# Performance work log

Measured on AMD Instinct MI355X. Metric: run time of the kernel, lower is better.

## Reference

```python
import jax, jax.numpy as jnp
import numpy as np

# Static config (mirrors XMem wrapper schedule)
B, T, H, W = 2, 16, 512, 512
P = 16                      # pad_divide_by(16) / stride-16 key encoder
h, w = H // P, W // P
HW = h * w
CK, CF, CV, CH = 64, 256, 512, 64   # key dim == hidden dim (XMem), f16 feat dim, value dim
MEM_EVERY, DEEP_EVERY = 5, 10
EPS = 1e-6


def setup_inputs() -> dict:
    key = jax.random.key(0)
    ks = jax.random.split(key, 12)
    def g(k, shape, s=0.02):
        return jax.random.normal(k, shape, jnp.float32) * s
    return {
        "frames": jax.random.normal(ks[0], (B, T, 3, H, W), jnp.float32),
        "init_masks": jax.random.uniform(ks[1], (B, 1, H, W), jnp.float32),
        "init_labels": jnp.ones((B, 1), jnp.int32),
        # key encoder (stride-16 patchify + linear projections, KeyProjection style)
        "W_key": g(ks[2], (3 * P * P, CK)),
        "W_shr": g(ks[3], (3 * P * P, 1)),
        "W_sel": g(ks[4], (3 * P * P, CK)),
        "W_f16": g(ks[5], (3 * P * P, CF)),
        # value encoder: concat(f16, mask) -> value; hidden update
        "W_val": g(ks[6], (CF + 1, CV)),
        "W_hid2": g(ks[7], (CV + CH, CH)),
        # decoder: concat(f16, readout, hidden) -> new hidden; -> fg logit
        "W_hd": g(ks[8], (CF + CV + CH, CH)),
        "W_dec": g(ks[9], (CF + CV + CH, 1)),
    }


def _patchify(img):  # [3,H,W] -> [HW, 3*P*P]
    x = img.reshape(3, h, P, w, P).transpose(1, 3, 0, 2, 4)
    return x.reshape(HW, 3 * P * P)


def _down(m):  # [H,W] -> [HW], average-pool by P (value-encoder mask downsample)
    return m.reshape(h, P, w, P).mean(axis=(1, 3)).reshape(HW)


def _aggregate(prob):  # XMem aggregate: prob [K,H,W] -> softmax([bg, fg...]) [K+1,H,W]
    bg = jnp.prod(1.0 - prob, axis=0, keepdims=True)
    newp = jnp.clip(jnp.concatenate([bg, prob], 0), 1e-7, 1.0 - 1e-7)
    logits = jnp.log(newp / (1.0 - newp))
    return jax.nn.softmax(logits, axis=0)


def _match(mk, ms, mv, qk, qe):
    # XMem get_similarity with shrinkage (ms) and selection (qe):
    # mk [CK,N], ms [N], mv [CV,N], qk/qe [CK,HW]
    a_sq = jnp.einsum('cn,cp->np', mk * mk, qe)
    two_ab = 2.0 * jnp.einsum('cn,cp->np', mk, qk * qe)
    b_sq = (qe * qk * qk).sum(0)                       # [HW]
    sim = (-a_sq + two_ab - b_sq) * ms[:, None] / np.sqrt(CK)
    aff = jax.nn.softmax(sim, axis=0)                  # softmax over memory entries
    return mv @ aff                                    # [CV, HW]


def _run_seq(frames_b, m0, Wk, Wsh, Wse, Wf, Wv, Wh2, Whd, Wdec):
    # frames_b [T,3,H,W], m0 [1,H,W]. H,W divisible by 16 so pad_divide_by is identity.
    patches = jax.vmap(_patchify)(frames_b)            # [T,HW,768]
    keys = patches @ Wk                                # [T,HW,CK]
    shrs = (patches @ Wsh) ** 2 + 1.0                  # [T,HW,1]  (d_proj**2 + 1)
    sels = jax.nn.sigmoid(patches @ Wse)               # [T,HW,CK]
    f16s = patches @ Wf                                # [T,HW,CF]

    mem_k, mem_s, mem_v = [], [], []
    hidden = jnp.zeros((HW, CH), jnp.float32)          # create_hidden_state
    last_mem, last_deep = 0, -DEEP_EVERY
    feats, masks = [], []
    for t in range(T):  # static schedule: mem frames and deep updates depend only on t
        is_mem = (t - last_mem >= MEM_EVERY or t == 0) and t != T - 1
        is_deep = (t - last_deep >= DEEP_EVERY) and t != T - 1
        qk, qe, f16 = keys[t].T, sels[t].T, f16s[t]    # qk,qe [CK,HW]
        ms_t = shrs[t][:, 0]
        pred_prob = None
        if t > 0:  # need_segment
            mk = jnp.concatenate(mem_k, 1)
            msv = jnp.concatenate(mem_s, 0)
            mv = jnp.concatenate(mem_v, 1)
            readout = _match(mk, msv, mv, qk, qe).T    # [HW,CV]
            hidden_local = jnp.tanh(jnp.concatenate([f16, readout, hidden], 1) @ Whd)
            fg = jnp.concatenate([f16, readout, hidden_local], 1) @ Wdec  # [HW,1]
            logits = jnp.concatenate([jnp.zeros((HW, 1), jnp.float32), fg], 1)
            pred_prob = jax.nn.softmax(logits, 1).T    # [2,HW] with bg
            if t != T - 1:                             # is_normal_update
                hidden = hidden_local
            m = pred_prob[1]
            feat = (hidden_local * m[:, None]).sum(0) / jnp.maximum(m.sum(), EPS)
            union = jax.image.resize(pred_prob[1].reshape(h, w), (H, W), 'bilinear')
        else:
            feat = keys[t].mean(0)                     # key.mean over spatial
            union = jnp.zeros((H, W), jnp.float32)
        feats.append(feat)
        masks.append(union)
        if is_mem:
            if t == 0:
                wprob = _aggregate(m0)                 # [2,H,W]
                wmask = _down(jax.lax.stop_gradient(wprob[1]))
            else:
                wmask = jax.lax.stop_gradient(pred_prob[1])
            value = jnp.concatenate([f16, wmask[:, None]], 1) @ Wv      # [HW,CV]
            hidden2 = jnp.tanh(jnp.concatenate([value, hidden], 1) @ Wh2)
            mem_k.append(qk)
            mem_s.append(ms_t)
            mem_v.append(value.T)
            last_mem = t
            if is_deep:
                hidden = hidden2
                last_deep = t
    return jnp.stack(feats, 0)                         # [T,CH]


def reference(frames, init_masks, init_labels, W_key, W_shr, W_sel, W_f16,
              W_val, W_hid2, W_hd, W_dec):
    del init_labels  # single-object labels [1]; no math
    run = lambda fb, mb: _run_seq(fb, mb, W_key, W_shr, W_sel, W_f16,
                                  W_val, W_hid2, W_hd, W_dec)
    return jax.vmap(run)(frames, init_masks)           # [B,T,CH]
```

## Files before the change

### kernel.cpp

```cpp
#include <hip/hip_runtime.h>
#include <cstdint>

typedef __bf16 bf16_t;
typedef __attribute__((ext_vector_type(8))) __bf16 bf16x8;
typedef __attribute__((ext_vector_type(4))) __bf16 bf16x4;
typedef __attribute__((ext_vector_type(4))) float f32x4;

#define MFMA16(a,b,c) __builtin_amdgcn_mfma_f32_16x16x32_bf16((a),(b),(c),0,0,0)

constexpr size_t PVSTR   = (size_t)2*5*1024*72;
constexpr size_t o_wcatT = 0;
constexpr size_t o_whfT  = o_wcatT + 172032;
constexpr size_t o_wvhT  = o_whfT  + 16384;
constexpr size_t o_wvh1  = o_wvhT  + 10240;
constexpr size_t o_WvT   = o_wvh1  + 80;
constexpr size_t o_whh   = o_WvT   + 65536;
constexpr size_t o_wh2T  = o_whh   + 4224;
constexpr size_t o_keyb  = o_wh2T  + 18432;
constexpr size_t o_ms    = o_keyb  + 1048576;
constexpr size_t o_qeb   = o_ms    + 32768;
constexpr size_t o_f16b  = o_qeb   + 1048576;
constexpr size_t o_qfb   = o_f16b  + 4194304;
constexpr size_t o_kfb   = o_qfb   + 2621440;
constexpr size_t o_vb    = o_kfb   + 491520;
constexpr size_t o_vhT   = o_vb    + 1572864;
constexpr size_t o_pv    = o_vhT   + 393216;
constexpr size_t o_p16   = o_pv    + 12*PVSTR;
constexpr size_t o_mh    = o_p16   + 1179648;
constexpr size_t o_hid   = o_mh    + 2027520;
constexpr size_t o_wmk   = o_hid   + 131072;
constexpr size_t ws_need = o_wmk   + 2048;

__global__ __launch_bounds__(256)
void k_init(const float* __restrict__ Wk, const float* __restrict__ Wsh,
            const float* __restrict__ Wse, const float* __restrict__ Wf,
            const float* __restrict__ Wv, const float* __restrict__ Wh2,
            const float* __restrict__ Whd, const float* __restrict__ Wdec,
            bf16_t* __restrict__ wcatT, bf16_t* __restrict__ whfT,
            bf16_t* __restrict__ WvT, float* __restrict__ whh,
            bf16_t* __restrict__ wh2T, float* __restrict__ out,
            bf16_t* __restrict__ wvhT, float* __restrict__ wvh1)
{
    int idx = blockIdx.x*256 + threadIdx.x;
    if (idx < 344064) {
        int n = idx/768, k = idx%768;
        float v = 0.f;
        if (n < 64)       v = Wk[k*64+n];
        else if (n == 64) v = Wsh[k];
        else if (n < 129) v = Wse[k*64+(n-65)];
        else if (n < 385) v = Wf[k*256+(n-129)];
        wcatT[idx] = (bf16_t)v;
        return;
    }
    idx -= 344064;
    if (idx < 32768) {
        int c = idx/256, k = idx%256;
        float v = 0.f;
        if (c < 64) v = Whd[k*64+c]; else if (c == 64) v = Wdec[k];
        whfT[idx] = (bf16_t)v;
        return;
    }
    idx -= 32768;
    if (idx < 131072) {
        int n = idx/256, k = idx%256;
        WvT[idx] = (bf16_t)Wv[k*512+n];
        return;
    }
    idx -= 131072;
    if (idx < 4224) {
        int k = idx/66, c = idx%66;
        float v = 0.f;
        if (c < 64) v = Whd[(768+k)*64+c]; else if (c == 64) v = Wdec[768+k];
        whh[idx] = v;
        return;
    }
    idx -= 4224;
    if (idx < 36864) {
        int c = idx/576, k = idx%576;
        wh2T[idx] = (bf16_t)Wh2[k*64+c];
        return;
    }
    idx -= 36864;
    if (idx < 128) {
        int b = idx>>6, c = idx&63;
        out[(size_t)b*1024 + c] = 0.f;
        return;
    }
    idx -= 128;
    if (idx < 20480) {
        int k = idx / 80, c = idx % 80;
        float s = 0.f;
        if (c < 65) {
            for (int j = 0; j < 512; j++) {
                float hv = (c < 64) ? Whd[(256+j)*64 + c] : Wdec[256 + j];
                s = fmaf(Wv[k*512 + j], hv, s);
            }
        }
        wvhT[(size_t)c*256 + k] = (bf16_t)s;
        return;
    }
    idx -= 20480;
    if (idx < 65) {
        int c = idx;
        float s = 0.f;
        for (int j = 0; j < 512; j++) {
            float hv = (c < 64) ? Whd[(256+j)*64 + c] : Wdec[256 + j];
            s = fmaf(Wv[256*512 + j], hv, s);
        }
        wvh1[c] = s;
    }
}

__global__ __launch_bounds__(512)
void k_proj(const float* __restrict__ frames, const bf16_t* __restrict__ wcatT,
            bf16_t* __restrict__ keyb, float* __restrict__ msb,
            bf16_t* __restrict__ qeb, bf16_t* __restrict__ f16b)
{
    const int bx = blockIdx.x, bt = blockIdx.y;
    const int p0 = bx*64;
    const int tid = threadIdx.x, lane = tid & 63, w = tid >> 6;
    const int wp = w >> 2, wn = w & 3;
    const int l15 = lane & 15, l4 = lane >> 4;
    __shared__ __align__(16) bf16_t Al[2][4][512];
    f32x4 acc[2][7] = {};
    const float* fb = frames + (size_t)bt*786432;

    const int lr = tid >> 7, lxb = (tid & 127)*8;
    const float* gbase = fb + (size_t)((bx*2 + (lr>>1))*16 + (lr&1))*512 + (tid & 127)*4;
    const int wbyte = lr*1024 + (lxb ^ (((lxb>>7)&3)<<4));
    const int rb_in = l15*32 + (l4&1)*16;
    const int rbyte = (wp*2 + (l4>>1))*1024 + (rb_in ^ (((rb_in>>7)&3)<<4));
    char* lds = (char*)&Al[0][0][0];

    #define PLOAD(dst, kc) dst = *(const float4*)(gbase + (size_t)((kc)>>3)*262144 + (size_t)(((kc)&7)*2)*512)
    #define PSTORE(buf, v) { bf16x4 pk; pk[0]=(bf16_t)(v).x; pk[1]=(bf16_t)(v).y; \
        pk[2]=(bf16_t)(v).z; pk[3]=(bf16_t)(v).w; \
        *(bf16x4*)(lds + (buf)*4096 + wbyte) = pk; }
    #define LBAR() { asm volatile("s_waitcnt lgkmcnt(0)" ::: "memory"); \
        __builtin_amdgcn_sched_barrier(0); \
        __builtin_amdgcn_s_barrier(); \
        __builtin_amdgcn_sched_barrier(0); }

    float4 va, vb;
    PLOAD(va, 0); PLOAD(vb, 1);
    PSTORE(0, va); PLOAD(va, 2);
    PSTORE(1, vb); PLOAD(vb, 3);
    LBAR();

    for (int kc = 0; kc < 24; kc++) {
        const int buf = kc & 1;
        bf16x8 af0 = *(const bf16x8*)(lds + buf*4096 + rbyte);
        bf16x8 af1 = *(const bf16x8*)(lds + buf*4096 + rbyte + 512);
        LBAR();
        if (kc < 22) {
            if (buf == 0) { PSTORE(0, va); if (kc < 20) PLOAD(va, kc+4); }
            else          { PSTORE(1, vb); if (kc < 20) PLOAD(vb, kc+4); }
        }
        #pragma unroll
        for (int fj = 0; fj < 7; fj++) {
            int n = wn*112 + fj*16 + l15;
            bf16x8 bv = *(const bf16x8*)(wcatT + (size_t)n*768 + kc*32 + l4*8);
            acc[0][fj] = MFMA16(af0, bv, acc[0][fj]);
            acc[1][fj] = MFMA16(af1, bv, acc[1][fj]);
        }
    }
    #undef PLOAD
    #undef PSTORE
    #undef LBAR

    #pragma unroll
    for (int fi = 0; fi < 2; fi++)
    #pragma unroll
    for (int fj = 0; fj < 7; fj++) {
        int nn = wn*112 + fj*16 + l15;
        #pragma unroll
        for (int rr = 0; rr < 4; rr++) {
            int pp = p0 + wp*32 + fi*16 + l4*4 + rr;
            float v = acc[fi][fj][rr];
            size_t rowb = (size_t)bt*1024 + pp;
            if (nn < 64)       keyb[rowb*64 + nn] = (bf16_t)v;
            else if (nn == 64) msb[rowb] = v*v + 1.f;
            else if (nn < 129) qeb[rowb*64 + (nn-65)] = (bf16_t)(1.f/(1.f+expf(-v)));
            else if (nn < 385) f16b[rowb*256 + (nn-129)] = (bf16_t)v;
        }
    }
}

__global__ __launch_bounds__(512)
void k_qf(const bf16_t* __restrict__ keyb, const bf16_t* __restrict__ qeb,
          bf16_t* __restrict__ qfb, float* __restrict__ out)
{
    int bt = blockIdx.x;
    int p = blockIdx.y*8 + threadIdx.y;
    int c = threadIdx.x;
    size_t rowb = (size_t)bt*1024 + p;
    float qk = (float)keyb[rowb*64 + c];
    float qv = (float)qeb[rowb*64 + c];
    float bsq = qv*qk*qk;
    #pragma unroll
    for (int off = 32; off; off >>= 1) bsq += __shfl_xor(bsq, off);
    bf16_t* q = qfb + rowb*160;
    q[c]      = (bf16_t)(qv*qk);
    q[64 + c] = (bf16_t)qv;
    if (c == 0) q[128] = (bf16_t)bsq;
    if (c < 31) q[129 + c] = (bf16_t)0.f;
    if ((bt & 15) == 0) {
        __shared__ float fred[64];
        if (threadIdx.y == 0) fred[c] = 0.f;
        __syncthreads();
        atomicAdd(&fred[c], qk);
        __syncthreads();
        if (threadIdx.y == 0)
            atomicAdd(&out[(size_t)(bt >> 4)*1024 + c], fred[c]*(1.f/1024.f));
    }
}

__global__ __launch_bounds__(256)
void k_mask0(const float* __restrict__ im, float* __restrict__ wmask)
{
    int blk = blockIdx.x;
    int b = blk >> 5, i = blk & 31;
    int tid = threadIdx.x;
    int xq = tid & 127, yh = tid >> 7;
    const float* base = im + (size_t)b*262144 + (size_t)(i*16)*512;
    float s = 0.f;
    for (int yy = 0; yy < 8; yy++) {
        int y = yy*2 + yh;
        float4 v = *(const float4*)(base + (size_t)y*512 + xq*4);
        float e[4] = {v.x, v.y, v.z, v.w};
        #pragma unroll
        for (int u = 0; u < 4; u++) {
            float pc = fminf(fmaxf(e[u],      1e-7f), 1.f-1e-7f);
            float qc = fminf(fmaxf(1.f-e[u],  1e-7f), 1.f-1e-7f);
            s += pc*pc/(pc*pc + qc*qc);
        }
    }
    __shared__ float red[32];
    if (tid < 32) red[tid] = 0.f;
    __syncthreads();
    atomicAdd(&red[xq >> 2], s);
    __syncthreads();
    if (tid < 32) wmask[b*1024 + i*32 + tid] = red[tid]*(1.f/256.f);
}

__global__ __launch_bounds__(128)
void k_prep(const bf16_t* __restrict__ f16b, const bf16_t* __restrict__ keyb,
            const float* __restrict__ msb, const float* __restrict__ wmk,
            const bf16_t* __restrict__ wvhT, const float* __restrict__ wvh1,
            bf16_t* __restrict__ kfb, bf16_t* __restrict__ vhT, int tm, int slot)
{
    int b = blockIdx.y, n0 = blockIdx.x*32;
    int tid = threadIdx.x, lane = tid & 63, w = tid >> 6;
    {
        int row = n0 + (tid >> 2), q = tid & 3;
        size_t rowb = (size_t)(b*16 + tm)*1024 + row;
        float m = msb[rowb];
        bf16_t* kr = kfb + ((size_t)b*3072 + slot*1024 + row)*160;
        bf16x8 k0v = *(const bf16x8*)(keyb + rowb*64 + q*16);
        bf16x8 k1v = *(const bf16x8*)(keyb + rowb*64 + q*16 + 8);
        bf16x8 o0, o1, s0, s1;
        #pragma unroll
        for (int u = 0; u < 8; u++) {
            float mk0 = (float)k0v[u], mk1 = (float)k1v[u];
            o0[u] = (bf16_t)( m*mk0*0.25f);       o1[u] = (bf16_t)( m*mk1*0.25f);
            s0[u] = (bf16_t)(-m*mk0*mk0*0.125f);  s1[u] = (bf16_t)(-m*mk1*mk1*0.125f);
        }
        *(bf16x8*)(kr + q*16)      = o0;  *(bf16x8*)(kr + q*16 + 8)      = o1;
        *(bf16x8*)(kr + 64 + q*16) = s0;  *(bf16x8*)(kr + 64 + q*16 + 8) = s1;
        if (q == 0) kr[128] = (bf16_t)(-m*0.125f);
        else if (q == 1) { for (int u = 0; u < 15; u++) kr[129+u] = (bf16_t)0.f; }
        else if (q == 2) { for (int u = 0; u < 16; u++) kr[144+u] = (bf16_t)0.f; }
    }
    int l15 = lane & 15, l4 = lane >> 4;
    const bf16_t* A = f16b + ((size_t)(b*16 + tm)*1024 + n0 + w*16 + l15)*256;
    f32x4 acc[5] = {};
    #pragma unroll
    for (int ks = 0; ks < 8; ks++) {
        bf16x8 a0 = *(const bf16x8*)(A + ks*32 + l4*8);
        #pragma unroll
        for (int cf = 0; cf < 5; cf++) {
            bf16x8 bv = *(const bf16x8*)(wvhT + (size_t)(cf*16 + l15)*256 + ks*32 + l4*8);
            acc[cf] = MFMA16(a0, bv, acc[cf]);
        }
    }
    #pragma unroll
    for (int cf = 0; cf < 5; cf++) {
        int cc = cf*16 + l15;
        float w1 = (cc < 65) ? wvh1[cc] : 0.f;
        #pragma unroll
        for (int rr = 0; rr < 4; rr++) {
            int p = n0 + w*16 + l4*4 + rr;
            float val;
            if (cc < 65)      val = acc[cf][rr] + wmk[b*1024 + p]*w1;
            else              val = (cc == 65) ? 1.f : 0.f;
            vhT[(size_t)b*393216 + (size_t)cc*3072 + slot*1024 + p] = (bf16_t)val;
        }
    }
}

__global__ __launch_bounds__(256)
void k_value(const bf16_t* __restrict__ f16b, const float* __restrict__ wmk,
             const bf16_t* __restrict__ WvT, const float* __restrict__ Wv,
             bf16_t* __restrict__ vb, int t, int slot)
{
    int b = blockIdx.z;
    int n0 = blockIdx.x*64, p0 = blockIdx.y*64;
    const int tid = threadIdx.x, lane = tid & 63, w = tid >> 6;
    const int wr = w >> 1, wc = w & 1, l15 = lane & 15, l4 = lane >> 4;
    const bf16_t* A = f16b + ((size_t)(b*16 + t)*1024 + p0)*256;
    f32x4 acc[2][2] = {};
    int ar = wr*32 + l15, bc = n0 + wc*32 + l15, koff = l4*8;
    #pragma unroll
    for (int ks = 0; ks < 8; ks++) {
        bf16x8 a0 = *(const bf16x8*)(A + (size_t)ar*256 + ks*32 + koff);
        bf16x8 a1 = *(const bf16x8*)(A + (size_t)(ar+16)*256 + ks*32 + koff);
        bf16x8 b0 = *(const bf16x8*)(WvT + (size_t)bc*256 + ks*32 + koff);
        bf16x8 b1 = *(const bf16x8*)(WvT + (size_t)(bc+16)*256 + ks*32 + koff);
        acc[0][0] = MFMA16(a0, b0, acc[0][0]);
        acc[0][1] = MFMA16(a0, b1, acc[0][1]);
        acc[1][0] = MFMA16(a1, b0, acc[1][0]);
        acc[1][1] = MFMA16(a1, b1, acc[1][1]);
    }
    #pragma unroll
    for (int fi = 0; fi < 2; fi++)
    #pragma unroll
    for (int fj = 0; fj < 2; fj++) {
        int nn = n0 + wc*32 + fj*16 + l15;
        float wvl = Wv[131072 + nn];
        #pragma unroll
        for (int rr = 0; rr < 4; rr++) {
            int pp = p0 + wr*32 + fi*16 + l4*4 + rr;
            float wm = wmk[b*1024 + pp];
            vb[((size_t)b*3072 + slot*1024 + pp)*512 + nn] = (bf16_t)(acc[fi][fj][rr] + wm*wvl);
        }
    }
}

__global__ __launch_bounds__(256)
void k_pre16(const bf16_t* __restrict__ f16b, const bf16_t* __restrict__ whfT,
             bf16_t* __restrict__ p16b)
{
    int bt = blockIdx.y;
    int p0 = blockIdx.x*64;
    const int tid = threadIdx.x, lane = tid & 63, w = tid >> 6;
    const int wr = w >> 1, wc = w & 1, l15 = lane & 15, l4 = lane >> 4;
    const bf16_t* A = f16b + ((size_t)bt*1024 + p0)*256;
    f32x4 acc[2][4] = {};
    int ar = wr*32 + l15, koff = l4*8;
    #pragma unroll
    for (int ks = 0; ks < 8; ks++) {
        bf16x8 a0 = *(const bf16x8*)(A + (size_t)ar*256 + ks*32 + koff);
        bf16x8 a1 = *(const bf16x8*)(A + (size_t)(ar+16)*256 + ks*32 + koff);
        #pragma unroll
        for (int fj = 0; fj < 4; fj++) {
            int cc = wc*64 + fj*16 + l15;
            bf16x8 bv = *(const bf16x8*)(whfT + (size_t)cc*256 + ks*32 + koff);
            acc[0][fj] = MFMA16(a0, bv, acc[0][fj]);
            acc[1][fj] = MFMA16(a1, bv, acc[1][fj]);
        }
    }
    #pragma unroll
    for (int fi = 0; fi < 2; fi++)
    #pragma unroll
    for (int fj = 0; fj < 4; fj++) {
        int cc = wc*64 + fj*16 + l15;
        if (cc < 65) {
            #pragma unroll
            for (int rr = 0; rr < 4; rr++) {
                int pp = p0 + wr*32 + fi*16 + l4*4 + rr;
                p16b[((size_t)bt*1024 + pp)*72 + cc] = (bf16_t)acc[fi][fj][rr];
            }
        }
    }
}

__global__ __launch_bounds__(256)
void k_att(const bf16_t* __restrict__ qfb, const bf16_t* __restrict__ kfb,
           const bf16_t* __restrict__ vhT, float* __restrict__ PVp, int t0)
{
    int b = blockIdx.z & 1, sl = blockIdx.z >> 1;
    int ts = blockIdx.y, t = t0 + ts, p0 = blockIdx.x*64;
    int n_base = sl*256;
    int tid = threadIdx.x, lane = tid & 63, w = tid >> 6;
    int l15 = lane & 15, l4 = lane >> 4;
    __shared__ __align__(16) bf16_t P_lds[4][16][72];

    const bf16_t* Q = qfb + ((size_t)(b*16 + t)*1024 + p0 + w*16 + l15)*160 + l4*8;
    bf16x8 aq[5];
    #pragma unroll
    for (int kc = 0; kc < 5; kc++) aq[kc] = *(const bf16x8*)(Q + kc*32);

    const bf16_t* K  = kfb + ((size_t)b*3072 + n_base)*160;
    const bf16_t* Vh = vhT + (size_t)b*393216 + n_base;
    f32x4 o[5] = {};

    for (int n0 = 0; n0 < 256; n0 += 64) {
        f32x4 s[4] = {};
        #pragma unroll
        for (int kc = 0; kc < 5; kc++) {
            #pragma unroll
            for (int nf = 0; nf < 4; nf++) {
                bf16x8 bk = *(const bf16x8*)(K + (size_t)(n0 + nf*16 + l15)*160 + kc*32 + l4*8);
                s[nf] = MFMA16(aq[kc], bk, s[nf]);
            }
        }
        #pragma unroll
        for (int nf = 0; nf < 4; nf++) {
            #pragma unroll
            for (int rr = 0; rr < 4; rr++) {
                float pe = __expf(s[nf][rr]);
                P_lds[w][l4*4 + rr][nf*16 + l15] = (bf16_t)pe;
            }
        }
        #pragma unroll
        for (int kc2 = 0; kc2 < 2; kc2++) {
            bf16x8 ap = *(const bf16x8*)&P_lds[w][l15][kc2*32 + l4*8];
            #pragma unroll
            for (int cf = 0; cf < 5; cf++) {
                bf16x8 bv = *(const bf16x8*)(Vh + (size_t)(cf*16 + l15)*3072 + n0 + kc2*32 + l4*8);
                o[cf] = MFMA16(ap, bv, o[cf]);
            }
        }
    }
    float* O = PVp + (size_t)sl*PVSTR + ((size_t)((b*5 + ts)*1024) + p0 + w*16)*72;
    #pragma unroll
    for (int cf = 0; cf < 5; cf++) {
        int cc = cf*16 + l15;
        if (cc < 66) {
            #pragma unroll
            for (int rr = 0; rr < 4; rr++)
                O[(size_t)(l4*4 + rr)*72 + cc] = o[cf][rr];
        }
    }
}

__global__ __launch_bounds__(256)
void k_chain2(const bf16_t* __restrict__ p16b, const float* __restrict__ PVp,
              const float* __restrict__ whhbuf, float* __restrict__ hidden,
              float* __restrict__ wmk, float* __restrict__ mh, int t0, int ph, int ns)
{
    int b = blockIdx.y;
    int tid = threadIdx.x, lane = tid & 63, w = tid >> 6;
    int p = blockIdx.x*4 + w;
    __shared__ float whh_s[64][66];
    __shared__ float hid_s[4][64];
    for (int idx = tid; idx < 64*66; idx += 256) whh_s[idx/66][idx%66] = whhbuf[idx];
    float h = hidden[((size_t)b*1024 + p)*64 + lane];
    hid_s[w][lane] = h;
    __syncthreads();
    float wd = whh_s[lane][64];
    for (int ts = 0; ts < 5; ts++) {
        int t = t0 + ts;
        size_t r16 = ((size_t)(b*16 + t)*1024 + p)*72;
        size_t rpv = ((size_t)((b*5 + ts)*1024) + p)*72;
        float pvc = 0.f, pv64 = 0.f, pv65 = 0.f;
        for (int s2 = 0; s2 < ns; s2++) {
            const float* bp = PVp + (size_t)s2*PVSTR + rpv;
            pvc  += bp[lane];
            pv64 += bp[64];
            pv65 += bp[65];
        }
        float rinv  = 1.f/pv65;
        float pre   = (float)p16b[r16 + lane] + pvc*rinv;
        float fgpre = (float)p16b[r16 + 64]   + pv64*rinv;
        float s = pre;
        #pragma unroll 8
        for (int k = 0; k < 64; k++) s += hid_s[w][k]*whh_s[k][lane];
        float hl = tanhf(s);
        float fgs = hl*wd;
        #pragma unroll
        for (int off = 1; off < 64; off <<= 1) fgs += __shfl_xor(fgs, off);
        float fg = fgpre + fgs;
        float m = 1.f/(1.f+expf(-fg));
        size_t rmh = ((size_t)(b*15 + ph*5 + ts)*1024 + p)*66;
        mh[rmh + lane] = m*hl;
        if (lane == 0) mh[rmh + 64] = m;
        if (ts == 4 && lane == 0) wmk[b*1024 + p] = m;
        h = hl;
        __syncthreads();
        hid_s[w][lane] = h;
        __syncthreads();
    }
    hidden[((size_t)b*1024 + p)*64 + lane] = h;
}

__global__ __launch_bounds__(256)
void k_hidm(const bf16_t* __restrict__ vb, const bf16_t* __restrict__ wh2T,
            float* __restrict__ hidden, int vslot, int has_h)
{
    int b = blockIdx.y, p0 = blockIdx.x*64;
    int tid = threadIdx.x, lane = tid & 63, w = tid >> 6;
    int l15 = lane & 15, l4 = lane >> 4;
    int arow = p0 + w*16 + l15;
    const bf16_t* A = vb + ((size_t)b*3072 + vslot*1024 + arow)*512;
    const float* Hp = hidden + ((size_t)b*1024 + arow)*64;
    f32x4 acc[4] = {};
    int kiters = has_h ? 18 : 16;
    for (int ks = 0; ks < kiters; ks++) {
        bf16x8 a0;
        if (ks < 16) a0 = *(const bf16x8*)(A + ks*32 + l4*8);
        else {
            int ko = (ks-16)*32 + l4*8;
            float4 h0 = *(const float4*)(Hp + ko);
            float4 h1 = *(const float4*)(Hp + ko + 4);
            a0[0]=(bf16_t)h0.x; a0[1]=(bf16_t)h0.y; a0[2]=(bf16_t)h0.z; a0[3]=(bf16_t)h0.w;
            a0[4]=(bf16_t)h1.x; a0[5]=(bf16_t)h1.y; a0[6]=(bf16_t)h1.z; a0[7]=(bf16_t)h1.w;
        }
        #pragma unroll
        for (int cf = 0; cf < 4; cf++) {
            bf16x8 bv = *(const bf16x8*)(wh2T + (size_t)(cf*16 + l15)*576 + ks*32 + l4*8);
            acc[cf] = MFMA16(a0, bv, acc[cf]);
        }
    }
    #pragma unroll
    for (int cf = 0; cf < 4; cf++) {
        int cc = cf*16 + l15;
        #pragma unroll
        for (int rr = 0; rr < 4; rr++) {
            int p = p0 + w*16 + l4*4 + rr;
            hidden[((size_t)b*1024 + p)*64 + cc] = tanhf(acc[cf][rr]);
        }
    }
}

__global__ __launch_bounds__(256)
void k_feats(const float* __restrict__ mh, float* __restrict__ out)
{
    int slot = blockIdx.x, b = blockIdx.y, t = slot + 1;
    int tid = threadIdx.x, c = tid & 63, g = tid >> 6;
    const float* base = mh + (size_t)(b*15 + slot)*1024*66;
    float s = 0.f, sm = 0.f;
    for (int p = g; p < 1024; p += 4) {
        s += base[(size_t)p*66 + c];
        if (c == 0) sm += base[(size_t)p*66 + 64];
    }
    __shared__ float red[4][64];
    __shared__ float redm[4];
    red[g][c] = s;
    if (c == 0) redm[g] = sm;
    __syncthreads();
    if (g == 0) {
        float tot  = red[0][c] + red[1][c] + red[2][c] + red[3][c];
        float totm = redm[0] + redm[1] + redm[2] + redm[3];
        out[(size_t)(b*16 + t)*64 + c] = tot / fmaxf(totm, 1e-6f);
    }
}

extern "C" void kernel_launch(void* const* d_in, const int* in_sizes, int n_in,
                              void* d_out, int out_size, void* d_ws, size_t ws_size,
                              hipStream_t stream)
{
    (void)in_sizes; (void)n_in; (void)out_size;
    if (ws_size < ws_need*sizeof(float)) return;
    const float* frames = (const float*)d_in[0];
    const float* imask  = (const float*)d_in[1];
    const float* Wk   = (const float*)d_in[3];
    const float* Wsh  = (const float*)d_in[4];
    const float* Wse  = (const float*)d_in[5];
    const float* Wf   = (const float*)d_in[6];
    const float* Wv   = (const float*)d_in[7];
    const float* Wh2  = (const float*)d_in[8];
    const float* Whd  = (const float*)d_in[9];
    const float* Wdec = (const float*)d_in[10];
    float* out = (float*)d_out;
    float* ws  = (float*)d_ws;

    bf16_t* wcatT = (bf16_t*)(ws + o_wcatT);
    bf16_t* whfT  = (bf16_t*)(ws + o_whfT);
    bf16_t* wvhT  = (bf16_t*)(ws + o_wvhT);
    float*  wvh1  = ws + o_wvh1;
    bf16_t* WvT   = (bf16_t*)(ws + o_WvT);
    float*  whh   = ws + o_whh;
    bf16_t* wh2T  = (bf16_t*)(ws + o_wh2T);
    bf16_t* keyb  = (bf16_t*)(ws + o_keyb);
    float*  msb   = ws + o_ms;
    bf16_t* qeb   = (bf16_t*)(ws + o_qeb);
    bf16_t* f16b  = (bf16_t*)(ws + o_f16b);
    bf16_t* qfb   = (bf16_t*)(ws + o_qfb);
    bf16_t* kfb   = (bf16_t*)(ws + o_kfb);
    bf16_t* vb    = (bf16_t*)(ws + o_vb);
    bf16_t* vhT   = (bf16_t*)(ws + o_vhT);
    float*  PVp   = ws + o_pv;
    bf16_t* p16b  = (bf16_t*)(ws + o_p16);
    float*  mh    = ws + o_mh;
    float*  hid   = ws + o_hid;
    float*  wmk   = ws + o_wmk;

    k_init<<<2226, 256, 0, stream>>>(Wk, Wsh, Wse, Wf, Wv, Wh2, Whd, Wdec,
                                     wcatT, whfT, WvT, whh, wh2T, out, wvhT, wvh1);
    k_proj<<<dim3(16,32), 512, 0, stream>>>(frames, wcatT, keyb, msb, qeb, f16b);
    k_qf<<<dim3(32,128), dim3(64,8), 0, stream>>>(keyb, qeb, qfb, out);
    k_mask0<<<64, 256, 0, stream>>>(imask, wmk);
    k_prep<<<dim3(32,2), 128, 0, stream>>>(f16b, keyb, msb, wmk, wvhT, wvh1, kfb, vhT, 0, 0);
    k_value<<<dim3(8,16,2), 256, 0, stream>>>(f16b, wmk, WvT, Wv, vb, 0, 0);
    k_hidm<<<dim3(16,2), 256, 0, stream>>>(vb, wh2T, hid, 0, 0);
    k_pre16<<<dim3(16,32), 256, 0, stream>>>(f16b, whfT, p16b);

    for (int ph = 0; ph < 3; ph++) {
        int t0 = 1 + ph*5;
        int ns = (ph + 1)*4;
        k_att<<<dim3(16,5,2*ns), 256, 0, stream>>>(qfb, kfb, vhT, PVp, t0);
        k_chain2<<<dim3(256,2), 256, 0, stream>>>(p16b, PVp, whh, hid, wmk, mh, t0, ph, ns);
        if (ph < 2) {
            int tm = t0 + 4, slot = ph + 1;
            k_prep<<<dim3(32,2), 128, 0, stream>>>(f16b, keyb, msb, wmk, wvhT, wvh1, kfb, vhT, tm, slot);
            if (ph == 1) {
                k_value<<<dim3(8,16,2), 256, 0, stream>>>(f16b, wmk, WvT, Wv, vb, tm, slot);
                k_hidm<<<dim3(16,2), 256, 0, stream>>>(vb, wh2T, hid, 2, 1);
            }
        }
    }
    k_feats<<<dim3(15,2), 256, 0, stream>>>(mh, out);
}
```

Measured before the change: 535.1 us.

## Process two frames per projection block and stage K/V tiles in LDS for attention

k_proj now handles two frames per block. Each weight fragment loaded from global memory feeds four MFMAs instead of two, and the grid is halved. k_att now loads each 64-key K tile and its V tile cooperatively into shared memory, so the four waves no longer each read K and V from global memory. The cost is more accumulator registers in k_proj, fewer blocks in flight, and two extra barriers per tile in k_att.

Measured after the change: 431.9 us. 19.3% less time.

```diff
diff --git a/kernel.cpp b/kernel.cpp
--- a/kernel.cpp
+++ b/kernel.cpp
@@ -116,52 +116,67 @@
             bf16_t* __restrict__ keyb, float* __restrict__ msb,
             bf16_t* __restrict__ qeb, bf16_t* __restrict__ f16b)
 {
-    const int bx = blockIdx.x, bt = blockIdx.y;
+    const int bx = blockIdx.x, btp = blockIdx.y;
     const int p0 = bx*64;
     const int tid = threadIdx.x, lane = tid & 63, w = tid >> 6;
     const int wp = w >> 2, wn = w & 3;
     const int l15 = lane & 15, l4 = lane >> 4;
-    __shared__ __align__(16) bf16_t Al[2][4][512];
-    f32x4 acc[2][7] = {};
-    const float* fb = frames + (size_t)bt*786432;
+    __shared__ __align__(16) bf16_t Al[2][2][4][512];
+    f32x4 acc[2][2][7] = {};
+    const float* fb0 = frames + (size_t)(btp*2)*786432;
+    const float* fb1 = fb0 + 786432;
 
     const int lr = tid >> 7, lxb = (tid & 127)*8;
-    const float* gbase = fb + (size_t)((bx*2 + (lr>>1))*16 + (lr&1))*512 + (tid & 127)*4;
+    const size_t grow = (size_t)((bx*2 + (lr>>1))*16 + (lr&1))*512 + (tid & 127)*4;
+    const float* gbase0 = fb0 + grow;
+    const float* gbase1 = fb1 + grow;
     const int wbyte = lr*1024 + (lxb ^ (((lxb>>7)&3)<<4));
     const int rb_in = l15*32 + (l4&1)*16;
     const int rbyte = (wp*2 + (l4>>1))*1024 + (rb_in ^ (((rb_in>>7)&3)<<4));
-    char* lds = (char*)&Al[0][0][0];
-
-    #define PLOAD(dst, kc) dst = *(const float4*)(gbase + (size_t)((kc)>>3)*262144 + (size_t)(((kc)&7)*2)*512)
-    #define PSTORE(buf, v) { bf16x4 pk; pk[0]=(bf16_t)(v).x; pk[1]=(bf16_t)(v).y; \
+    char* lds = (char*)&Al[0][0][0][0];
+
+    #define PLOAD(dst, gb, kc) dst = *(const float4*)((gb) + (size_t)((kc)>>3)*262144 + (size_t)(((kc)&7)*2)*512)
+    #define PSTORE(f, buf, v) { bf16x4 pk; pk[0]=(bf16_t)(v).x; pk[1]=(bf16_t)(v).y; \
         pk[2]=(bf16_t)(v).z; pk[3]=(bf16_t)(v).w; \
-        *(bf16x4*)(lds + (buf)*4096 + wbyte) = pk; }
+        *(bf16x4*)(lds + (f)*8192 + (buf)*4096 + wbyte) = pk; }
     #define LBAR() { asm volatile("s_waitcnt lgkmcnt(0)" ::: "memory"); \
         __builtin_amdgcn_sched_barrier(0); \
         __builtin_amdgcn_s_barrier(); \
         __builtin_amdgcn_sched_barrier(0); }
 
-    float4 va, vb;
-    PLOAD(va, 0); PLOAD(vb, 1);
-    PSTORE(0, va); PLOAD(va, 2);
-    PSTORE(1, vb); PLOAD(vb, 3);
+    float4 va0, vb0, va1, vb1;
+    PLOAD(va0, gbase0, 0); PLOAD(va1, gbase1, 0);
+    PLOAD(vb0, gbase0, 1); PLOAD(vb1, gbase1, 1);
+    PSTORE(0, 0, va0); PSTORE(1, 0, va1);
+    PLOAD(va0, gbase0, 2); PLOAD(va1, gbase1, 2);
+    PSTORE(0, 1, vb0); PSTORE(1, 1, vb1);
+    PLOAD(vb0, gbase0, 3); PLOAD(vb1, gbase1, 3);
     LBAR();
 
     for (int kc = 0; kc < 24; kc++) {
         const int buf = kc & 1;
-        bf16x8 af0 = *(const bf16x8*)(lds + buf*4096 + rbyte);
-        bf16x8 af1 = *(const bf16x8*)(lds + buf*4096 + rbyte + 512);
+        bf16x8 a00 = *(const bf16x8*)(lds + buf*4096 + rbyte);
+        bf16x8 a01 = *(const bf16x8*)(lds + buf*4096 + rbyte + 512);
+        bf16x8 a10 = *(const bf16x8*)(lds + 8192 + buf*4096 + rbyte);
+        bf16x8 a11 = *(const bf16x8*)(lds + 8192 + buf*4096 + rbyte + 512);
         LBAR();
         if (kc < 22) {
-            if (buf == 0) { PSTORE(0, va); if (kc < 20) PLOAD(va, kc+4); }
-            else          { PSTORE(1, vb); if (kc < 20) PLOAD(vb, kc+4); }
+            if (buf == 0) {
+                PSTORE(0, 0, va0); PSTORE(1, 0, va1);
+                if (kc < 20) { PLOAD(va0, gbase0, kc+4); PLOAD(va1, gbase1, kc+4); }
+            } else {
+                PSTORE(0, 1, vb0); PSTORE(1, 1, vb1);
+                if (kc < 20) { PLOAD(vb0, gbase0, kc+4); PLOAD(vb1, gbase1, kc+4); }
+            }
         }
         #pragma unroll
         for (int fj = 0; fj < 7; fj++) {
             int n = wn*112 + fj*16 + l15;
             bf16x8 bv = *(const bf16x8*)(wcatT + (size_t)n*768 + kc*32 + l4*8);
-            acc[0][fj] = MFMA16(af0, bv, acc[0][fj]);
-            acc[1][fj] = MFMA16(af1, bv, acc[1][fj]);
+            acc[0][0][fj] = MFMA16(a00, bv, acc[0][0][fj]);
+            acc[0][1][fj] = MFMA16(a01, bv, acc[0][1][fj]);
+            acc[1][0][fj] = MFMA16(a10, bv, acc[1][0][fj]);
+            acc[1][1][fj] = MFMA16(a11, bv, acc[1][1][fj]);
         }
     }
     #undef PLOAD
@@ -169,19 +184,23 @@
     #undef LBAR
 
     #pragma unroll
-    for (int fi = 0; fi < 2; fi++)
-    #pragma unroll
-    for (int fj = 0; fj < 7; fj++) {
-        int nn = wn*112 + fj*16 + l15;
-        #pragma unroll
-        for (int rr = 0; rr < 4; rr++) {
-            int pp = p0 + wp*32 + fi*16 + l4*4 + rr;
-            float v = acc[fi][fj][rr];
-            size_t rowb = (size_t)bt*1024 + pp;
-            if (nn < 64)       keyb[rowb*64 + nn] = (bf16_t)v;
-            else if (nn == 64) msb[rowb] = v*v + 1.f;
-            else if (nn < 129) qeb[rowb*64 + (nn-65)] = (bf16_t)(1.f/(1.f+expf(-v)));
-            else if (nn < 385) f16b[rowb*256 + (nn-129)] = (bf16_t)v;
+    for (int f = 0; f < 2; f++) {
+        int bt = btp*2 + f;
+        #pragma unroll
+        for (int fi = 0; fi < 2; fi++)
+        #pragma unroll
+        for (int fj = 0; fj < 7; fj++) {
+            int nn = wn*112 + fj*16 + l15;
+            #pragma unroll
+            for (int rr = 0; rr < 4; rr++) {
+                int pp = p0 + wp*32 + fi*16 + l4*4 + rr;
+                float v = acc[f][fi][fj][rr];
+                size_t rowb = (size_t)bt*1024 + pp;
+                if (nn < 64)       keyb[rowb*64 + nn] = (bf16_t)v;
+                else if (nn == 64) msb[rowb] = v*v + 1.f;
+                else if (nn < 129) qeb[rowb*64 + (nn-65)] = (bf16_t)(1.f/(1.f+expf(-v)));
+                else if (nn < 385) f16b[rowb*256 + (nn-129)] = (bf16_t)v;
+            }
         }
     }
 }
@@ -383,6 +402,8 @@
     int n_base = sl*256;
     int tid = threadIdx.x, lane = tid & 63, w = tid >> 6;
     int l15 = lane & 15, l4 = lane >> 4;
+    __shared__ __align__(16) bf16_t K_lds[64][168];
+    __shared__ __align__(16) bf16_t V_lds[80][72];
     __shared__ __align__(16) bf16_t P_lds[4][16][72];
 
     const bf16_t* Q = qfb + ((size_t)(b*16 + t)*1024 + p0 + w*16 + l15)*160 + l4*8;
@@ -390,17 +411,32 @@
     #pragma unroll
     for (int kc = 0; kc < 5; kc++) aq[kc] = *(const bf16x8*)(Q + kc*32);
 
-    const bf16_t* K  = kfb + ((size_t)b*3072 + n_base)*160;
-    const bf16_t* Vh = vhT + (size_t)b*393216 + n_base;
     f32x4 o[5] = {};
 
     for (int n0 = 0; n0 < 256; n0 += 64) {
+        const bf16_t* Ksrc = kfb + ((size_t)b*3072 + n_base + n0)*160;
+        #pragma unroll
+        for (int it = 0; it < 5; it++) {
+            int idx = it*256 + tid;
+            int row = idx/20, ch = idx%20;
+            *(bf16x8*)&K_lds[row][ch*8] = *(const bf16x8*)(Ksrc + (size_t)row*160 + ch*8);
+        }
+        const bf16_t* Vsrc = vhT + (size_t)b*393216 + n_base + n0;
+        #pragma unroll
+        for (int it = 0; it < 3; it++) {
+            int idx = it*256 + tid;
+            if (idx < 640) {
+                int row = idx >> 3, ch = idx & 7;
+                *(bf16x8*)&V_lds[row][ch*8] = *(const bf16x8*)(Vsrc + (size_t)row*3072 + ch*8);
+            }
+        }
+        __syncthreads();
         f32x4 s[4] = {};
         #pragma unroll
         for (int kc = 0; kc < 5; kc++) {
             #pragma unroll
             for (int nf = 0; nf < 4; nf++) {
-                bf16x8 bk = *(const bf16x8*)(K + (size_t)(n0 + nf*16 + l15)*160 + kc*32 + l4*8);
+                bf16x8 bk = *(const bf16x8*)&K_lds[nf*16 + l15][kc*32 + l4*8];
                 s[nf] = MFMA16(aq[kc], bk, s[nf]);
             }
         }
@@ -417,10 +453,11 @@
             bf16x8 ap = *(const bf16x8*)&P_lds[w][l15][kc2*32 + l4*8];
             #pragma unroll
             for (int cf = 0; cf < 5; cf++) {
-                bf16x8 bv = *(const bf16x8*)(Vh + (size_t)(cf*16 + l15)*3072 + n0 + kc2*32 + l4*8);
+                bf16x8 bv = *(const bf16x8*)&V_lds[cf*16 + l15][kc2*32 + l4*8];
                 o[cf] = MFMA16(ap, bv, o[cf]);
             }
         }
+        __syncthreads();
     }
     float* O = PVp + (size_t)sl*PVSTR + ((size_t)((b*5 + ts)*1024) + p0 + w*16)*72;
     #pragma unroll
@@ -588,7 +625,7 @@
 
     k_init<<<2226, 256, 0, stream>>>(Wk, Wsh, Wse, Wf, Wv, Wh2, Whd, Wdec,
                                      wcatT, whfT, WvT, whh, wh2T, out, wvhT, wvh1);
-    k_proj<<<dim3(16,32), 512, 0, stream>>>(frames, wcatT, keyb, msb, qeb, f16b);
+    k_proj<<<dim3(16,16), 512, 0, stream>>>(frames, wcatT, keyb, msb, qeb, f16b);
     k_qf<<<dim3(32,128), dim3(64,8), 0, stream>>>(keyb, qeb, qfb, out);
     k_mask0<<<64, 256, 0, stream>>>(imask, wmk);
     k_prep<<<dim3(32,2), 128, 0, stream>>>(f16b, keyb, msb, wmk, wvhT, wvh1, kfb, vhT, 0, 0);
```
